# Kernel tuning notes

Hardware: AMD Instinct MI355X
Metric: run time of the kernel (lower is better)

Reference implementation:

```python
import jax, jax.numpy as jnp
import numpy as np

N = 1536       # n_nodes
D_IN = 256     # in_features
D_OUT = 64     # out_features (= n_hidden, n_heads=1, is_concat=True)
N_WAY = 16     # known_attacks_count
SLOPE = 0.2    # LeakyReLU negative slope


def setup_inputs() -> dict:
    key = jax.random.key(0)
    k1, k2, k3, k4, k5 = jax.random.split(key, 5)
    hidden_vectors = jax.random.normal(k1, (N, D_IN), dtype=jnp.float32)
    labels = jax.random.randint(k2, (N, 1), 0, N_WAY)
    zda_mask = jax.random.randint(k3, (N, 1), 0, 2).astype(bool)
    # deterministic support/query split: first half support, last half query
    query_mask = jnp.concatenate([jnp.zeros(N // 2, bool), jnp.ones(N // 2, bool)])
    W = jax.random.normal(k4, (D_OUT, D_IN), jnp.float32) * (1.0 / np.sqrt(D_IN))
    attn_w = jax.random.normal(k5, (D_OUT,), jnp.float32) * (1.0 / np.sqrt(D_OUT))
    return {"hidden_vectors": hidden_vectors, "W": W, "attn_w": attn_w,
            "labels": labels, "zda_mask": zda_mask, "query_mask": query_mask,
            "known_attacks_count": N_WAY}


def _forward(hidden_vectors, W, attn_w, labels, zda_mask, n_way):
    n = hidden_vectors.shape[0]
    dt = hidden_vectors.dtype
    # one-hot labels (scatter equivalent)
    oh = jax.nn.one_hot(labels[:, 0], n_way, dtype=dt)                 # [n, n_way]
    known = ~zda_mask[:, 0]                                            # unknown == zda
    ohm = jnp.where(known[:, None], oh, jnp.zeros((), dt))             # masked one-hot
    # collaborative kernel: semantic similarity between known pairs, else 1
    sem = ohm @ ohm.T                                                  # [n, n]
    cond = known[:, None] & known[None, :]
    kernel = jnp.where(cond, sem, jnp.ones((), dt))
    # GATv2 with shared weights, 1 head: e[i,j] = attn . lrelu(g[i] + g[j])
    g = hidden_vectors @ W.T                                           # [n, d_out]
    s = g[:, None, :] + g[None, :, :]                                  # [n, n, d_out]
    s = jnp.where(s >= 0, s, SLOPE * s)                                # LeakyReLU
    e = jnp.einsum('ijd,d->ij', s, attn_w)                             # [n, n]
    e = jnp.where(kernel == 0.0, -jnp.inf, e)                          # colaborative mask
    a = jax.nn.softmax(e, axis=1)                                      # [n, n]
    h_out = a @ g                                                      # [n, d_out] (concat, 1 head)
    # centroids over support nodes (first half)
    n_sup = n // 2
    h_sup, oh_sup = h_out[:n_sup], oh[:n_sup]
    agg = oh_sup.T @ h_sup                                             # [n_way, d_out]
    counts = oh_sup.sum(0)                                             # [n_way]
    centroids = jnp.where((counts > 0)[:, None],
                          agg / jnp.maximum(counts, 1.0)[:, None], 0.0)
    # inverse euclidean distance scores for query nodes (last half)
    hq = h_out[n_sup:]
    d2 = (jnp.sum(hq * hq, 1)[:, None] + jnp.sum(centroids * centroids, 1)[None, :]
          - 2.0 * hq @ centroids.T)
    dist = jnp.sqrt(jnp.maximum(d2, 0.0))
    scores = 1.0 / (dist + 1e-10)
    return scores, h_out, a


def reference(hidden_vectors, W, attn_w, labels, zda_mask, query_mask, known_attacks_count):
    return _forward(hidden_vectors, W, attn_w, labels, zda_mask, known_attacks_count)
```

## Files before the change

kernel.cpp:

```cpp
#include <hip/hip_runtime.h>
#include <math.h>

#define NN 1536
#define DIN 256
#define DOUT 64
#define NWAY 16
#define NSUP 768
#define IB 12
#define JBLK 128

#define OFF_SCORES 0
#define OFF_H 12288
#define OFF_A 110592

#define WG 0
#define WQ 98304
#define WCODE 99840
#define WCENT 101376
#define WHP 102400

__global__ __launch_bounds__(256) void k_g(const float* __restrict__ hid,
                                           const float* __restrict__ W,
                                           const float* __restrict__ attw,
                                           const int* __restrict__ labels,
                                           const int* __restrict__ zda,
                                           float* __restrict__ g,
                                           float* __restrict__ q,
                                           int* __restrict__ code) {
  int t = threadIdx.x;
  int r = t >> 6, d = t & 63;
  int i = blockIdx.x * 4 + r;
  const float4* hp = (const float4*)(hid + (size_t)i * DIN);
  const float4* wp = (const float4*)(W + (size_t)d * DIN);
  float4 acc = {0.f, 0.f, 0.f, 0.f};
#pragma unroll
  for (int k = 0; k < DIN / 4; k++) {
    float4 h4 = hp[k];
    float4 w4 = wp[k];
    acc.x = fmaf(h4.x, w4.x, acc.x);
    acc.y = fmaf(h4.y, w4.y, acc.y);
    acc.z = fmaf(h4.z, w4.z, acc.z);
    acc.w = fmaf(h4.w, w4.w, acc.w);
  }
  float gv = (acc.x + acc.y) + (acc.z + acc.w);
  g[(size_t)i * DOUT + d] = gv;
  float val = gv * attw[d];
#pragma unroll
  for (int off = 32; off >= 1; off >>= 1) val += __shfl_xor(val, off, 64);
  if (d == 0) q[i] = 0.6f * val;
  if (t < 4) {
    int ii = blockIdx.x * 4 + t;
    code[ii] = zda[ii] ? -1 : labels[ii];
  }
}

__global__ __launch_bounds__(256, 3) void k_e(const float* __restrict__ g,
                                              const float* __restrict__ q,
                                              const int* __restrict__ code,
                                              const float* __restrict__ attw,
                                              float* __restrict__ aout) {
  __shared__ float gis[IB * DOUT];
  __shared__ float lds_p[4][IB][64];
  __shared__ float qi[IB];
  __shared__ int ci[IB];
  int t = threadIdx.x;
  int lane = t & 63;
  int w = t >> 6;
  int whalf = __builtin_amdgcn_readfirstlane(w & 1);
  int jhi = w >> 1;
  int i0 = blockIdx.x * IB;
  int j0 = blockIdx.y * JBLK;
  int j = j0 + jhi * 64 + lane;

  if (t < IB * 16) {
    ((float4*)gis)[t] = ((const float4*)(g + (size_t)i0 * DOUT))[t];
  } else if (t < IB * 16 + IB) {
    int u = t - IB * 16;
    qi[u] = q[i0 + u];
    ci[u] = code[i0 + u];
  }
  float4 gj[8];
  const float4* gp = (const float4*)(g + (size_t)j * DOUT + whalf * 32);
#pragma unroll
  for (int k = 0; k < 8; k++) gj[k] = gp[k];
  const float4* wv = (const float4*)(attw + whalf * 32);
  __syncthreads();

#pragma unroll 1
  for (int u = 0; u < IB; u++) {
    const float4* gv = (const float4*)(gis + u * DOUT + whalf * 32);
    float4 acc = {0.f, 0.f, 0.f, 0.f};
#pragma unroll
    for (int k = 0; k < 8; k++) {
      float4 a4 = gv[k];
      float4 w4 = wv[k];
      float4 b4 = gj[k];
      acc.x = fmaf(w4.x, fabsf(a4.x + b4.x), acc.x);
      acc.y = fmaf(w4.y, fabsf(a4.y + b4.y), acc.y);
      acc.z = fmaf(w4.z, fabsf(a4.z + b4.z), acc.z);
      acc.w = fmaf(w4.w, fabsf(a4.w + b4.w), acc.w);
    }
    lds_p[w][u][lane] = (acc.x + acc.y) + (acc.z + acc.w);
  }
  __syncthreads();

  int jl = t & 127;
  int sb = (jl >> 6) * 2;
  int ll = jl & 63;
  int jg = j0 + jl;
  float qj = q[jg];
  int cj = code[jg];
  int u0 = (t >> 7) * 6;
#pragma unroll
  for (int v = 0; v < 6; v++) {
    int u = u0 + v;
    float s = lds_p[sb][u][ll] + lds_p[sb + 1][u][ll];
    float e = (qi[u] + qj) + 0.4f * s;
    int cu = ci[u];
    if ((cu >= 0) && (cj >= 0) && (cu != cj)) e = -1e30f;
    aout[(size_t)(i0 + u) * NN + jg] = e;
  }
}

__global__ __launch_bounds__(256) void k_sm(float* __restrict__ a) {
  __shared__ float red[8];
  int i = blockIdx.x, t = threadIdx.x;
  float* row = a + (size_t)i * NN;
  float v[6];
#pragma unroll
  for (int k = 0; k < 6; k++) v[k] = row[t + 256 * k];
  float m = v[0];
#pragma unroll
  for (int k = 1; k < 6; k++) m = fmaxf(m, v[k]);
#pragma unroll
  for (int off = 32; off >= 1; off >>= 1) m = fmaxf(m, __shfl_xor(m, off, 64));
  int w = t >> 6;
  if ((t & 63) == 0) red[w] = m;
  __syncthreads();
  m = fmaxf(fmaxf(red[0], red[1]), fmaxf(red[2], red[3]));
  float s = 0.f;
#pragma unroll
  for (int k = 0; k < 6; k++) {
    v[k] = __expf(v[k] - m);
    s += v[k];
  }
#pragma unroll
  for (int off = 32; off >= 1; off >>= 1) s += __shfl_xor(s, off, 64);
  if ((t & 63) == 0) red[4 + w] = s;
  __syncthreads();
  s = (red[4] + red[5]) + (red[6] + red[7]);
  float inv = 1.f / s;
#pragma unroll
  for (int k = 0; k < 6; k++) row[t + 256 * k] = v[k] * inv;
}

__global__ __launch_bounds__(256) void k_h(const float* __restrict__ a,
                                           const float* __restrict__ g,
                                           float* __restrict__ hp) {
  __shared__ float at[16 * 132];
  __shared__ float gl[128 * 64];
  int t = threadIdx.x;
  int jc = blockIdx.y;
  int r0 = blockIdx.x * 16;
#pragma unroll
  for (int u = 0; u < 2; u++) {
    int f4 = t + u * 256;
    int row = f4 >> 5;
    int col4 = f4 & 31;
    float4 v = *(const float4*)(a + (size_t)(r0 + row) * NN + jc * 128 + col4 * 4);
    *(float4*)(at + row * 132 + col4 * 4) = v;
  }
  {
    const float4* src = (const float4*)(g + (size_t)jc * 128 * DOUT);
    float4* dst = (float4*)gl;
#pragma unroll
    for (int u = 0; u < 8; u++) dst[t + u * 256] = src[t + u * 256];
  }
  __syncthreads();
  int r = t >> 4;
  int dq = (t & 15) * 4;
  const float4* ap = (const float4*)(at + r * 132);
  float4 acc = {0.f, 0.f, 0.f, 0.f};
  for (int j4 = 0; j4 < 32; j4++) {
    float4 av = ap[j4];
    const float* gb = gl + (j4 * 4) * 64 + dq;
    float4 g0 = *(const float4*)(gb);
    float4 g1 = *(const float4*)(gb + 64);
    float4 g2 = *(const float4*)(gb + 128);
    float4 g3 = *(const float4*)(gb + 192);
    acc.x = fmaf(av.x, g0.x, acc.x); acc.y = fmaf(av.x, g0.y, acc.y);
    acc.z = fmaf(av.x, g0.z, acc.z); acc.w = fmaf(av.x, g0.w, acc.w);
    acc.x = fmaf(av.y, g1.x, acc.x); acc.y = fmaf(av.y, g1.y, acc.y);
    acc.z = fmaf(av.y, g1.z, acc.z); acc.w = fmaf(av.y, g1.w, acc.w);
    acc.x = fmaf(av.z, g2.x, acc.x); acc.y = fmaf(av.z, g2.y, acc.y);
    acc.z = fmaf(av.z, g2.z, acc.z); acc.w = fmaf(av.z, g2.w, acc.w);
    acc.x = fmaf(av.w, g3.x, acc.x); acc.y = fmaf(av.w, g3.y, acc.y);
    acc.z = fmaf(av.w, g3.z, acc.z); acc.w = fmaf(av.w, g3.w, acc.w);
  }
  *(float4*)(hp + ((size_t)jc * NN + r0 + r) * DOUT + dq) = acc;
}

__global__ __launch_bounds__(256) void k_hred(const float* __restrict__ hp,
                                              float* __restrict__ h) {
  int idx = blockIdx.x * 256 + threadIdx.x;
  float s = 0.f;
#pragma unroll
  for (int c = 0; c < 12; c++) s += hp[(size_t)c * (NN * DOUT) + idx];
  h[idx] = s;
}

__global__ __launch_bounds__(1024) void k_cent(const float* __restrict__ h,
                                               const int* __restrict__ labels,
                                               float* __restrict__ cent) {
  __shared__ float part[16][64];
  __shared__ int pc[16];
  int c = blockIdx.x, t = threadIdx.x;
  int d = t & 63, rq = t >> 6;
  float acc = 0.f;
  int cnt = 0;
#pragma unroll 4
  for (int r = rq; r < NSUP; r += 16) {
    int lab = labels[r];
    if (lab == c) { acc += h[(size_t)r * DOUT + d]; cnt++; }
  }
  part[rq][d] = acc;
  if (d == 0) pc[rq] = cnt;
  __syncthreads();
  if (t < 64) {
    float num = 0.f;
    int count = 0;
#pragma unroll
    for (int k = 0; k < 16; k++) { num += part[k][t]; count += pc[k]; }
    cent[c * DOUT + t] = (count > 0) ? (num / (float)count) : 0.f;
  }
}

__global__ __launch_bounds__(256) void k_scores(const float* __restrict__ h,
                                                const float* __restrict__ cent,
                                                float* __restrict__ scores) {
  __shared__ float cl[NWAY * 65];
  __shared__ float hl[16 * 65];
  int t = threadIdx.x;
  int q0 = blockIdx.x * 16;
#pragma unroll
  for (int u = 0; u < 4; u++) {
    int f = t + u * 256;
    int row = f >> 6, k = f & 63;
    cl[row * 65 + k] = cent[f];
    hl[row * 65 + k] = h[(size_t)(NSUP + q0) * DOUT + f];
  }
  __syncthreads();
  int qr = t >> 4, c = t & 15;
  const float* hv = hl + qr * 65;
  const float* cv = cl + c * 65;
  float hh = 0.f, cc = 0.f, hc = 0.f;
#pragma unroll
  for (int k = 0; k < DOUT; k++) {
    float av = hv[k], bv = cv[k];
    hh = fmaf(av, av, hh);
    cc = fmaf(bv, bv, cc);
    hc = fmaf(av, bv, hc);
  }
  float d2 = fmaxf(hh + cc - 2.f * hc, 0.f);
  scores[q0 * NWAY + t] = 1.f / (sqrtf(d2) + 1e-10f);
}

extern "C" void kernel_launch(void* const* d_in, const int* in_sizes, int n_in,
                              void* d_out, int out_size, void* d_ws, size_t ws_size,
                              hipStream_t stream) {
  const float* hid = (const float*)d_in[0];
  const float* W = (const float*)d_in[1];
  const float* attw = (const float*)d_in[2];
  const int* labels = (const int*)d_in[3];
  const int* zda = (const int*)d_in[4];
  float* out = (float*)d_out;
  float* ws = (float*)d_ws;

  float* g = ws + WG;
  float* q = ws + WQ;
  int* code = (int*)(ws + WCODE);
  float* cent = ws + WCENT;
  float* hp = ws + WHP;
  float* scores = out + OFF_SCORES;
  float* h = out + OFF_H;
  float* a = out + OFF_A;

  hipLaunchKernelGGL(k_g, dim3(NN / 4), dim3(256), 0, stream, hid, W, attw, labels, zda, g, q, code);
  hipLaunchKernelGGL(k_e, dim3(NN / IB, NN / JBLK), dim3(256), 0, stream, g, q, code, attw, a);
  hipLaunchKernelGGL(k_sm, dim3(NN), dim3(256), 0, stream, a);
  hipLaunchKernelGGL(k_h, dim3(NN / 16, NN / 128), dim3(256), 0, stream, a, g, hp);
  hipLaunchKernelGGL(k_hred, dim3(NN * DOUT / 256), dim3(256), 0, stream, hp, h);
  hipLaunchKernelGGL(k_cent, dim3(NWAY), dim3(1024), 0, stream, h, labels, cent);
  hipLaunchKernelGGL(k_scores, dim3(NSUP / 16), dim3(256), 0, stream, h, cent, scores);
}
```

Measured before the change: 77.62 us.

## Fuse row softmax with attention-weighted aggregation into one kernel

Merges the softmax, the split-K a@g product and the partial-sum reduction into a single kernel. Each 512-thread block normalizes 6 rows, keeps them in LDS, then multiplies them against g read from global/L2. This removes the re-read of the 9 MB attention matrix, the partial buffer and two launches. In exchange there are only 256 blocks with large LDS use, and g is streamed per block, so per-block work is more serial.

```diff
diff --git a/kernel.cpp b/kernel.cpp
--- a/kernel.cpp
+++ b/kernel.cpp
@@ -8,6 +8,7 @@
 #define NSUP 768
 #define IB 12
 #define JBLK 128
+#define SROWS 6
 
 #define OFF_SCORES 0
 #define OFF_H 12288
@@ -17,7 +18,6 @@
 #define WQ 98304
 #define WCODE 99840
 #define WCENT 101376
-#define WHP 102400
 
 __global__ __launch_bounds__(256) void k_g(const float* __restrict__ hid,
                                            const float* __restrict__ W,
@@ -122,91 +122,84 @@
   }
 }
 
-__global__ __launch_bounds__(256) void k_sm(float* __restrict__ a) {
-  __shared__ float red[8];
-  int i = blockIdx.x, t = threadIdx.x;
-  float* row = a + (size_t)i * NN;
-  float v[6];
-#pragma unroll
-  for (int k = 0; k < 6; k++) v[k] = row[t + 256 * k];
-  float m = v[0];
-#pragma unroll
-  for (int k = 1; k < 6; k++) m = fmaxf(m, v[k]);
-#pragma unroll
-  for (int off = 32; off >= 1; off >>= 1) m = fmaxf(m, __shfl_xor(m, off, 64));
+__global__ __launch_bounds__(512) void k_smh(float* __restrict__ a,
+                                             const float* __restrict__ g,
+                                             float* __restrict__ h) {
+  __shared__ float al[SROWS][NN];
+  __shared__ float part[32][SROWS][68];
+  __shared__ float red[16];
+  int t = threadIdx.x;
+  int lane = t & 63;
   int w = t >> 6;
-  if ((t & 63) == 0) red[w] = m;
-  __syncthreads();
-  m = fmaxf(fmaxf(red[0], red[1]), fmaxf(red[2], red[3]));
-  float s = 0.f;
-#pragma unroll
-  for (int k = 0; k < 6; k++) {
-    v[k] = __expf(v[k] - m);
-    s += v[k];
-  }
-#pragma unroll
-  for (int off = 32; off >= 1; off >>= 1) s += __shfl_xor(s, off, 64);
-  if ((t & 63) == 0) red[4 + w] = s;
-  __syncthreads();
-  s = (red[4] + red[5]) + (red[6] + red[7]);
-  float inv = 1.f / s;
-#pragma unroll
-  for (int k = 0; k < 6; k++) row[t + 256 * k] = v[k] * inv;
-}
-
-__global__ __launch_bounds__(256) void k_h(const float* __restrict__ a,
-                                           const float* __restrict__ g,
-                                           float* __restrict__ hp) {
-  __shared__ float at[16 * 132];
-  __shared__ float gl[128 * 64];
-  int t = threadIdx.x;
-  int jc = blockIdx.y;
-  int r0 = blockIdx.x * 16;
-#pragma unroll
-  for (int u = 0; u < 2; u++) {
-    int f4 = t + u * 256;
-    int row = f4 >> 5;
-    int col4 = f4 & 31;
-    float4 v = *(const float4*)(a + (size_t)(r0 + row) * NN + jc * 128 + col4 * 4);
-    *(float4*)(at + row * 132 + col4 * 4) = v;
-  }
-  {
-    const float4* src = (const float4*)(g + (size_t)jc * 128 * DOUT);
-    float4* dst = (float4*)gl;
-#pragma unroll
-    for (int u = 0; u < 8; u++) dst[t + u * 256] = src[t + u * 256];
-  }
-  __syncthreads();
-  int r = t >> 4;
-  int dq = (t & 15) * 4;
-  const float4* ap = (const float4*)(at + r * 132);
-  float4 acc = {0.f, 0.f, 0.f, 0.f};
-  for (int j4 = 0; j4 < 32; j4++) {
-    float4 av = ap[j4];
-    const float* gb = gl + (j4 * 4) * 64 + dq;
-    float4 g0 = *(const float4*)(gb);
-    float4 g1 = *(const float4*)(gb + 64);
-    float4 g2 = *(const float4*)(gb + 128);
-    float4 g3 = *(const float4*)(gb + 192);
-    acc.x = fmaf(av.x, g0.x, acc.x); acc.y = fmaf(av.x, g0.y, acc.y);
-    acc.z = fmaf(av.x, g0.z, acc.z); acc.w = fmaf(av.x, g0.w, acc.w);
-    acc.x = fmaf(av.y, g1.x, acc.x); acc.y = fmaf(av.y, g1.y, acc.y);
-    acc.z = fmaf(av.y, g1.z, acc.z); acc.w = fmaf(av.y, g1.w, acc.w);
-    acc.x = fmaf(av.z, g2.x, acc.x); acc.y = fmaf(av.z, g2.y, acc.y);
-    acc.z = fmaf(av.z, g2.z, acc.z); acc.w = fmaf(av.z, g2.w, acc.w);
-    acc.x = fmaf(av.w, g3.x, acc.x); acc.y = fmaf(av.w, g3.y, acc.y);
-    acc.z = fmaf(av.w, g3.z, acc.z); acc.w = fmaf(av.w, g3.w, acc.w);
-  }
-  *(float4*)(hp + ((size_t)jc * NN + r0 + r) * DOUT + dq) = acc;
-}
-
-__global__ __launch_bounds__(256) void k_hred(const float* __restrict__ hp,
-                                              float* __restrict__ h) {
-  int idx = blockIdx.x * 256 + threadIdx.x;
-  float s = 0.f;
-#pragma unroll
-  for (int c = 0; c < 12; c++) s += hp[(size_t)c * (NN * DOUT) + idx];
-  h[idx] = s;
+  int r0 = blockIdx.x * SROWS;
+
+#pragma unroll 1
+  for (int r = 0; r < SROWS; r++) {
+    float* row = a + (size_t)(r0 + r) * NN;
+    float v0 = row[t], v1 = row[t + 512], v2 = row[t + 1024];
+    float m = fmaxf(fmaxf(v0, v1), v2);
+#pragma unroll
+    for (int off = 32; off >= 1; off >>= 1) m = fmaxf(m, __shfl_xor(m, off, 64));
+    if (lane == 0) red[w] = m;
+    __syncthreads();
+    m = red[0];
+#pragma unroll
+    for (int k = 1; k < 8; k++) m = fmaxf(m, red[k]);
+    v0 = __expf(v0 - m);
+    v1 = __expf(v1 - m);
+    v2 = __expf(v2 - m);
+    float s = (v0 + v1) + v2;
+#pragma unroll
+    for (int off = 32; off >= 1; off >>= 1) s += __shfl_xor(s, off, 64);
+    if (lane == 0) red[8 + w] = s;
+    __syncthreads();
+    s = red[8];
+#pragma unroll
+    for (int k = 1; k < 8; k++) s += red[8 + k];
+    float inv = 1.f / s;
+    v0 *= inv; v1 *= inv; v2 *= inv;
+    al[r][t] = v0; al[r][t + 512] = v1; al[r][t + 1024] = v2;
+    row[t] = v0; row[t + 512] = v1; row[t + 1024] = v2;
+    __syncthreads();
+  }
+
+  int jr = t >> 4;
+  int dq = t & 15;
+  float4 acc0 = {0,0,0,0}, acc1 = {0,0,0,0}, acc2 = {0,0,0,0};
+  float4 acc3 = {0,0,0,0}, acc4 = {0,0,0,0}, acc5 = {0,0,0,0};
+#pragma unroll 4
+  for (int jj = 0; jj < NN / 32; jj++) {
+    int j = jj * 32 + jr;
+    float4 g4 = *(const float4*)(g + (size_t)j * DOUT + dq * 4);
+    float a0 = al[0][j], a1 = al[1][j], a2 = al[2][j];
+    float a3 = al[3][j], a4 = al[4][j], a5 = al[5][j];
+    acc0.x = fmaf(a0, g4.x, acc0.x); acc0.y = fmaf(a0, g4.y, acc0.y);
+    acc0.z = fmaf(a0, g4.z, acc0.z); acc0.w = fmaf(a0, g4.w, acc0.w);
+    acc1.x = fmaf(a1, g4.x, acc1.x); acc1.y = fmaf(a1, g4.y, acc1.y);
+    acc1.z = fmaf(a1, g4.z, acc1.z); acc1.w = fmaf(a1, g4.w, acc1.w);
+    acc2.x = fmaf(a2, g4.x, acc2.x); acc2.y = fmaf(a2, g4.y, acc2.y);
+    acc2.z = fmaf(a2, g4.z, acc2.z); acc2.w = fmaf(a2, g4.w, acc2.w);
+    acc3.x = fmaf(a3, g4.x, acc3.x); acc3.y = fmaf(a3, g4.y, acc3.y);
+    acc3.z = fmaf(a3, g4.z, acc3.z); acc3.w = fmaf(a3, g4.w, acc3.w);
+    acc4.x = fmaf(a4, g4.x, acc4.x); acc4.y = fmaf(a4, g4.y, acc4.y);
+    acc4.z = fmaf(a4, g4.z, acc4.z); acc4.w = fmaf(a4, g4.w, acc4.w);
+    acc5.x = fmaf(a5, g4.x, acc5.x); acc5.y = fmaf(a5, g4.y, acc5.y);
+    acc5.z = fmaf(a5, g4.z, acc5.z); acc5.w = fmaf(a5, g4.w, acc5.w);
+  }
+  *(float4*)(&part[jr][0][dq * 4]) = acc0;
+  *(float4*)(&part[jr][1][dq * 4]) = acc1;
+  *(float4*)(&part[jr][2][dq * 4]) = acc2;
+  *(float4*)(&part[jr][3][dq * 4]) = acc3;
+  *(float4*)(&part[jr][4][dq * 4]) = acc4;
+  *(float4*)(&part[jr][5][dq * 4]) = acc5;
+  __syncthreads();
+  if (t < SROWS * DOUT) {
+    int r = t >> 6, d = t & 63;
+    float s = 0.f;
+#pragma unroll
+    for (int k = 0; k < 32; k++) s += part[k][r][d];
+    h[(size_t)(r0 + r) * DOUT + d] = s;
+  }
 }
 
 __global__ __launch_bounds__(1024) void k_cent(const float* __restrict__ h,
@@ -280,16 +273,13 @@
   float* q = ws + WQ;
   int* code = (int*)(ws + WCODE);
   float* cent = ws + WCENT;
-  float* hp = ws + WHP;
   float* scores = out + OFF_SCORES;
   float* h = out + OFF_H;
   float* a = out + OFF_A;
 
   hipLaunchKernelGGL(k_g, dim3(NN / 4), dim3(256), 0, stream, hid, W, attw, labels, zda, g, q, code);
   hipLaunchKernelGGL(k_e, dim3(NN / IB, NN / JBLK), dim3(256), 0, stream, g, q, code, attw, a);
-  hipLaunchKernelGGL(k_sm, dim3(NN), dim3(256), 0, stream, a);
-  hipLaunchKernelGGL(k_h, dim3(NN / 16, NN / 128), dim3(256), 0, stream, a, g, hp);
-  hipLaunchKernelGGL(k_hred, dim3(NN * DOUT / 256), dim3(256), 0, stream, hp, h);
+  hipLaunchKernelGGL(k_smh, dim3(NN / SROWS), dim3(512), 0, stream, a, g, h);
   hipLaunchKernelGGL(k_cent, dim3(NWAY), dim3(1024), 0, stream, h, labels, cent);
   hipLaunchKernelGGL(k_scores, dim3(NSUP / 16), dim3(256), 0, stream, h, cent, scores);
 }
```

After: 72.01 us. 1.08x faster.
